# Optimization experiments

Measured on AMD Instinct MI355X. Metric: run time of the kernel, lower is better.

Reference implementation:

```python
import jax, jax.numpy as jnp
import numpy as np


def setup_inputs() -> dict:
    key = jax.random.key(0)
    ks = jax.random.split(key, 5)
    B, C, H, W = 16, 512, 64, 64
    cm = cn = C // 4  # int(C*0.5*0.5)
    # kaiming_normal fan_out for 1x1 conv: std = sqrt(2 / out_channels)
    def kaiming(k, out_c, in_c):
        return jax.random.normal(k, (out_c, in_c), jnp.float32) * np.sqrt(2.0 / out_c)
    return {
        "x": jax.random.normal(ks[0], (B, C, H, W), jnp.float32),
        "WA": kaiming(ks[1], cm, C), "bA": jnp.zeros((cm,), jnp.float32),
        "WB": kaiming(ks[2], cn, C), "bB": jnp.zeros((cn,), jnp.float32),
        "WV": kaiming(ks[3], cn, C), "bV": jnp.zeros((cn,), jnp.float32),
        "WR": kaiming(ks[4], C, cm), "bR": jnp.zeros((C,), jnp.float32),
    }


def reference(x, WA, bA, WB, bB, WV, bV, WR, bR):
    b, c, h, w = x.shape
    n = h * w
    xf = x.reshape(b, c, n)  # [b, c, n] flattened spatial
    # 1x1 convs == per-pixel GEMMs
    A = jnp.einsum('mc,bcn->bmn', WA, xf) + bA[None, :, None]          # [b, cm, n]
    Bm = jax.nn.softmax(jnp.einsum('mc,bcn->bmn', WB, xf) + bB[None, :, None], axis=1)  # softmax over channels
    Vm = jax.nn.softmax(jnp.einsum('mc,bcn->bmn', WV, xf) + bV[None, :, None], axis=1)
    # second-order pooling: global descriptors [b, cm, cn]
    gd = jnp.einsum('bmn,bkn->bmk', A, Bm)
    # distribute: [b, cm, n]
    Z = jnp.einsum('bmk,bkn->bmn', gd, Vm)
    # reconstruct 1x1 conv back to c channels
    out = jnp.einsum('cm,bmn->bcn', WR, Z) + bR[None, :, None]
    return out.reshape(b, c, h, w)
```

## Files before the change

### kernel.cpp

```cpp
#include <hip/hip_runtime.h>
#include <hip/hip_fp16.h>


typedef _Float16 half8 __attribute__((ext_vector_type(8)));
typedef float f32x4 __attribute__((ext_vector_type(4)));

__device__ __forceinline__ unsigned short f2h(float v) {
  return __builtin_bit_cast(unsigned short, (_Float16)v);
}
__device__ __forceinline__ unsigned pk2(float a, float b) {
  return (unsigned)f2h(a) | ((unsigned)f2h(b) << 16);
}
__device__ __forceinline__ f32x4 mfma16(half8 a, half8 b, f32x4 c) {
  return __builtin_amdgcn_mfma_f32_16x16x32_f16(a, b, c, 0, 0, 0);
}
__device__ __forceinline__ int perm32(int v) {
  return (((v & 15) >> 2) << 3) | (((v >> 4) & 1) << 2) | (v & 3);
}
__device__ __forceinline__ void glds16(const unsigned short* g, unsigned short* l) {
  __builtin_amdgcn_global_load_lds(
      (const __attribute__((address_space(1))) unsigned int*)g,
      (__attribute__((address_space(3))) unsigned int*)l, 16, 0, 0);
}
__device__ __forceinline__ half8 ld_frag(const unsigned short* lds, int row) {
  int kg = (threadIdx.x & 63) >> 4;
  uint4 u = *(const uint4*)&lds[(kg * 128 + row) * 8];
  return __builtin_bit_cast(half8, u);
}
__device__ __forceinline__ half8 ld_frag64(const unsigned short* lds, int row) {
  int kg = (threadIdx.x & 63) >> 4;
  uint4 u = *(const uint4*)&lds[(kg * 64 + row) * 8];
  return __builtin_bit_cast(half8, u);
}

__device__ __forceinline__ void stage_glds256(unsigned short* lds,
                                              const unsigned short* g,
                                              int gs, int k0) {
  const int lane = threadIdx.x & 63;
  const int w = threadIdx.x >> 6;
#pragma unroll
  for (int p = 0; p < 2; ++p) {
    int g0 = (w + p * 4) * 64;
    int gi = g0 + lane;
    int row = gi & 127, kg = gi >> 7;
    glds16(g + (size_t)row * gs + k0 + kg * 8, lds + g0 * 8);
  }
}

__global__ __launch_bounds__(256) void k_prep(
    const float* __restrict__ WA, const float* __restrict__ WB,
    const float* __restrict__ WV, const float* __restrict__ WR,
    unsigned short* __restrict__ Wh, unsigned short* __restrict__ WRh) {
  int idx = blockIdx.x * 256 + threadIdx.x;
  if (idx < 196608) {
    int mg = idx >> 16, r = idx & 65535;
    const float* src = (mg == 0) ? WA : ((mg == 1) ? WB : WV);
    Wh[(idx & ~31) | perm32(idx & 31)] = f2h(src[r]);
  } else {
    int r = idx - 196608;
    WRh[(r & ~31) | perm32(r & 31)] = f2h(WR[r]);
  }
}

__global__ __launch_bounds__(384, 3) void k_abv_gd(
    const float* __restrict__ x, const unsigned short* __restrict__ Wh,
    const float* __restrict__ bA, const float* __restrict__ bB,
    const float* __restrict__ bV,
    unsigned short* __restrict__ VmT, float* __restrict__ gdP) {
  const int nt = blockIdx.x, b = blockIdx.y;
  const int tid = threadIdx.x, lane = tid & 63, w = tid >> 6;
  const int kg = lane >> 4, lidx = lane & 15;
  const int mg = w >> 1, wh = w & 1;

  __shared__ unsigned short smem[16384];
  __shared__ float cmaxs[2][2][64], csums[2][2][64];
  __shared__ float sBias[384];

  sBias[tid] = ((mg == 0) ? bA : ((mg == 1) ? bB : bV))[tid & 127];

  const float* xbase = x + (size_t)b * 512 * 4096 + nt * 64;
  const int xn = tid & 63;
  const int xkg = (tid >> 6) & 3;
  const bool xact = (tid < 256);

  float xr[8];

#define XLOAD(K0) do { \
  if (xact) { \
    _Pragma("unroll") for (int j = 0; j < 4; ++j) { \
      xr[j]     = xbase[(size_t)((K0) + 4 * xkg + j) * 4096 + xn]; \
      xr[4 + j] = xbase[(size_t)((K0) + 16 + 4 * xkg + j) * 4096 + xn]; \
    } } } while (0)

#define XWRITE(SX) do { \
  if (xact) { \
    uint4 u_; \
    u_.x = pk2(xr[0], xr[1]); u_.y = pk2(xr[2], xr[3]); \
    u_.z = pk2(xr[4], xr[5]); u_.w = pk2(xr[6], xr[7]); \
    *(uint4*)&(SX)[(xkg * 64 + xn) * 8] = u_; \
  } } while (0)

#define WLOAD(AF, K0) do { \
  _Pragma("unroll") for (int mf_ = 0; mf_ < 4; ++mf_) { \
    const unsigned short* wp_ = Wh + mg * 65536 + \
        (size_t)(wh * 64 + mf_ * 16 + lidx) * 512 + (K0) + kg * 8; \
    (AF)[mf_] = __builtin_bit_cast(half8, *(const uint4*)wp_); \
  } } while (0)

  f32x4 acc[4][4];
#pragma unroll
  for (int mf = 0; mf < 4; ++mf)
#pragma unroll
    for (int nf = 0; nf < 4; ++nf) acc[mf][nf] = (f32x4){0.f, 0.f, 0.f, 0.f};

  half8 afc[4], afn[4];

  XLOAD(0);
  WLOAD(afc, 0);
  XWRITE(smem);

  for (int ks = 0; ks < 16; ++ks) {
    unsigned short* cw = smem + (ks & 1) * 2048;
    unsigned short* nx = smem + ((ks & 1) ^ 1) * 2048;
    __syncthreads();
    if (ks < 15) {
      XLOAD((ks + 1) * 32);
      WLOAD(afn, (ks + 1) * 32);
    }
#pragma unroll
    for (int nf = 0; nf < 4; ++nf) {
      half8 bf = ld_frag64(cw, nf * 16 + lidx);
#pragma unroll
      for (int mf = 0; mf < 4; ++mf)
        acc[mf][nf] = mfma16(afc[mf], bf, acc[mf][nf]);
    }
    if (ks < 15) {
      XWRITE(nx);
#pragma unroll
      for (int mf = 0; mf < 4; ++mf) afc[mf] = afn[mf];
    }
  }

#pragma unroll
  for (int mf = 0; mf < 4; ++mf)
#pragma unroll
    for (int i = 0; i < 4; ++i) {
      float bb = sBias[mg * 128 + wh * 64 + mf * 16 + kg * 4 + i];
#pragma unroll
      for (int nf = 0; nf < 4; ++nf) acc[mf][nf][i] += bb;
    }

  float inv_s[4];
  if (mg) {
#pragma unroll
    for (int nf = 0; nf < 4; ++nf) {
      float m = -1e30f;
#pragma unroll
      for (int mf = 0; mf < 4; ++mf)
#pragma unroll
        for (int i = 0; i < 4; ++i) m = fmaxf(m, acc[mf][nf][i]);
      m = fmaxf(m, __shfl_xor(m, 16));
      m = fmaxf(m, __shfl_xor(m, 32));
      if (kg == 0) cmaxs[mg - 1][wh][nf * 16 + lidx] = m;
      inv_s[nf] = m;
    }
  }
  __syncthreads();
  if (mg) {
#pragma unroll
    for (int nf = 0; nf < 4; ++nf) {
      float m = fmaxf(inv_s[nf], cmaxs[mg - 1][wh ^ 1][nf * 16 + lidx]);
      float s = 0.f;
#pragma unroll
      for (int mf = 0; mf < 4; ++mf)
#pragma unroll
        for (int i = 0; i < 4; ++i) {
          float e = __expf(acc[mf][nf][i] - m);
          acc[mf][nf][i] = e;
          s += e;
        }
      s += __shfl_xor(s, 16);
      s += __shfl_xor(s, 32);
      if (kg == 0) csums[mg - 1][wh][nf * 16 + lidx] = s;
      inv_s[nf] = s;
    }
  }
  __syncthreads();
  if (mg) {
#pragma unroll
    for (int nf = 0; nf < 4; ++nf)
      inv_s[nf] = 1.f / (inv_s[nf] + csums[mg - 1][wh ^ 1][nf * 16 + lidx]);
  }

  unsigned short* sA2 = smem;
  unsigned short* sB2 = smem + 8192;

  __syncthreads();
  if (mg != 2) {
    unsigned short* dst = (mg == 0) ? sA2 : sB2;
#pragma unroll
    for (int nf = 0; nf < 4; ++nf) {
      int base = (nf >> 1) * 4096 + (lidx >> 2) * 1024 + (nf & 1) * 4 + (lidx & 3);
#pragma unroll
      for (int mf = 0; mf < 4; ++mf)
#pragma unroll
        for (int i = 0; i < 4; ++i) {
          int m_ = wh * 64 + mf * 16 + kg * 4 + i;
          float v = acc[mf][nf][i];
          dst[base + m_ * 8] = f2h(mg ? v * inv_s[nf] : v);
        }
    }
  } else {
    const size_t vofs = ((size_t)b * 4096 + (size_t)nt * 64) * 128;
#pragma unroll
    for (int mf = 0; mf < 4; ++mf) {
      int m0 = wh * 64 + mf * 16 + kg * 4;
      int mp = (m0 & ~31) + perm32(m0 & 31);
#pragma unroll
      for (int nf = 0; nf < 4; ++nf) {
        int n_ = nf * 16 + lidx;
        ushort4 pk;
        pk.x = f2h(acc[mf][nf][0] * inv_s[nf]);
        pk.y = f2h(acc[mf][nf][1] * inv_s[nf]);
        pk.z = f2h(acc[mf][nf][2] * inv_s[nf]);
        pk.w = f2h(acc[mf][nf][3] * inv_s[nf]);
        *(ushort4*)&VmT[vofs + (size_t)n_ * 128 + mp] = pk;
      }
    }
  }
  __syncthreads();

  if (mg != 2) {
    const int gr = wh, gc = mg;
    f32x4 g2[4][4];
#pragma unroll
    for (int mf = 0; mf < 4; ++mf)
#pragma unroll
      for (int nf = 0; nf < 4; ++nf) g2[mf][nf] = (f32x4){0.f, 0.f, 0.f, 0.f};
#pragma unroll
    for (int ks2 = 0; ks2 < 2; ++ks2) {
      half8 af2[4];
#pragma unroll
      for (int mf = 0; mf < 4; ++mf)
        af2[mf] = ld_frag(sA2 + ks2 * 4096, gr * 64 + mf * 16 + lidx);
#pragma unroll
      for (int nf = 0; nf < 4; ++nf) {
        half8 bf2 = ld_frag(sB2 + ks2 * 4096, gc * 64 + nf * 16 + lidx);
#pragma unroll
        for (int mf = 0; mf < 4; ++mf)
          g2[mf][nf] = mfma16(af2[mf], bf2, g2[mf][nf]);
      }
    }
    float* gp = gdP + ((size_t)b * 64 + nt) * 16384;
#pragma unroll
    for (int mf = 0; mf < 4; ++mf)
#pragma unroll
      for (int nf = 0; nf < 4; ++nf) {
        int m0 = gr * 64 + mf * 16 + kg * 4;
        int k2 = gc * 64 + nf * 16 + lidx;
        *(f32x4*)&gp[(size_t)k2 * 128 + m0] = g2[mf][nf];
      }
  }
#undef XLOAD
#undef XWRITE
#undef WLOAD
}

__global__ __launch_bounds__(256) void k_gdred(
    const float* __restrict__ gdP, float* __restrict__ gdT) {
  int gid = blockIdx.x * 256 + threadIdx.x;
  int o = gid * 4;
  int b = o >> 14, rem = o & 16383;
  const float* src = gdP + (size_t)b * 64 * 16384 + rem;
  f32x4 s = (f32x4){0.f, 0.f, 0.f, 0.f};
#pragma unroll 8
  for (int nt = 0; nt < 64; ++nt) s += *(const f32x4*)(src + (size_t)nt * 16384);
  *(f32x4*)(gdT + o) = s;
}

__global__ __launch_bounds__(256) void k_gw(
    const float* __restrict__ gdT, const unsigned short* __restrict__ WRh,
    unsigned short* __restrict__ GWh) {
  const int ct = blockIdx.x, b = blockIdx.y;
  const int tid = threadIdx.x, lane = tid & 63;
  const int w = tid >> 6, wr = w >> 1, wc = w & 1;
  const int kg = lane >> 4, lidx = lane & 15;
  __shared__ unsigned short sG[4096], sWr[4096];
  const float* gb = gdT + (size_t)b * 16384;
  const unsigned short* Wb = WRh + ct * 128 * 128;

  f32x4 acc[4][4];
#pragma unroll
  for (int mf = 0; mf < 4; ++mf)
#pragma unroll
    for (int nf = 0; nf < 4; ++nf) acc[mf][nf] = (f32x4){0.f, 0.f, 0.f, 0.f};

  for (int k0 = 0; k0 < 128; k0 += 32) {
#pragma unroll
    for (int p = 0; p < 2; ++p) {
      int g = tid + p * 256;
      int row = g & 127, kgx = g >> 7;
      const float* s0 = &gb[row * 128 + k0 + 4 * kgx];
      float4 v0 = *(const float4*)s0;
      float4 v1 = *(const float4*)(s0 + 16);
      uint4 u;
      u.x = pk2(v0.x, v0.y); u.y = pk2(v0.z, v0.w);
      u.z = pk2(v1.x, v1.y); u.w = pk2(v1.z, v1.w);
      *(uint4*)&sG[g * 8] = u;
    }
    stage_glds256(sWr, Wb, 128, k0);
    __syncthreads();
    half8 af[4];
#pragma unroll
    for (int mf = 0; mf < 4; ++mf) af[mf] = ld_frag(sG, wr * 64 + mf * 16 + lidx);
#pragma unroll
    for (int nf = 0; nf < 4; ++nf) {
      half8 bf = ld_frag(sWr, wc * 64 + nf * 16 + lidx);
#pragma unroll
      for (int mf = 0; mf < 4; ++mf) acc[mf][nf] = mfma16(af[mf], bf, acc[mf][nf]);
    }
    __syncthreads();
  }
  const size_t gofs = ((size_t)b * 512 + (size_t)ct * 128) * 128;
#pragma unroll
  for (int mf = 0; mf < 4; ++mf) {
    int k0g = wr * 64 + mf * 16 + kg * 4;
    int kp = (k0g & ~31) + perm32(k0g & 31);
#pragma unroll
    for (int nf = 0; nf < 4; ++nf) {
      int c_ = wc * 64 + nf * 16 + lidx;
      ushort4 pk;
      pk.x = f2h(acc[mf][nf][0]); pk.y = f2h(acc[mf][nf][1]);
      pk.z = f2h(acc[mf][nf][2]); pk.w = f2h(acc[mf][nf][3]);
      *(ushort4*)&GWh[gofs + (size_t)c_ * 128 + kp] = pk;
    }
  }
}

__global__ __launch_bounds__(256) void k_out(
    const unsigned short* __restrict__ GWh, const unsigned short* __restrict__ VmT,
    const float* __restrict__ bR, float* __restrict__ out) {
  const int nt = blockIdx.x, ct = blockIdx.y, b = blockIdx.z;
  const int tid = threadIdx.x, lane = tid & 63;
  const int w = tid >> 6, wr = w >> 1, wc = w & 1;
  const int kg = lane >> 4, lidx = lane & 15;
  __shared__ unsigned short sW[4096], sZ[4096];
  __shared__ float sBias[128];
  if (tid < 128) sBias[tid] = bR[ct * 128 + tid];
  const unsigned short* Wb = GWh + ((size_t)b * 512 + (size_t)ct * 128) * 128;
  const unsigned short* Zb = VmT + ((size_t)b * 4096 + (size_t)nt * 128) * 128;

  f32x4 acc[4][4];
#pragma unroll
  for (int mf = 0; mf < 4; ++mf)
#pragma unroll
    for (int nf = 0; nf < 4; ++nf) acc[mf][nf] = (f32x4){0.f, 0.f, 0.f, 0.f};

  for (int k0 = 0; k0 < 128; k0 += 32) {
    stage_glds256(sW, Wb, 128, k0);
    stage_glds256(sZ, Zb, 128, k0);
    __syncthreads();
    half8 af[4];
#pragma unroll
    for (int mf = 0; mf < 4; ++mf) af[mf] = ld_frag(sW, wr * 64 + mf * 16 + lidx);
#pragma unroll
    for (int nf = 0; nf < 4; ++nf) {
      half8 bf = ld_frag(sZ, wc * 64 + nf * 16 + lidx);
#pragma unroll
      for (int mf = 0; mf < 4; ++mf) acc[mf][nf] = mfma16(af[mf], bf, acc[mf][nf]);
    }
    __syncthreads();
  }
#pragma unroll
  for (int mf = 0; mf < 4; ++mf)
#pragma unroll
    for (int nf = 0; nf < 4; ++nf)
#pragma unroll
      for (int i = 0; i < 4; ++i) {
        int cl = wr * 64 + mf * 16 + kg * 4 + i;
        int n_ = nt * 128 + wc * 64 + nf * 16 + lidx;
        out[((size_t)b * 512 + ct * 128 + cl) * 4096 + n_] = acc[mf][nf][i] + sBias[cl];
      }
}

extern "C" void kernel_launch(void* const* d_in, const int* in_sizes, int n_in,
                              void* d_out, int out_size, void* d_ws, size_t ws_size,
                              hipStream_t stream) {
  const float* x  = (const float*)d_in[0];
  const float* WA = (const float*)d_in[1];
  const float* bA = (const float*)d_in[2];
  const float* WB = (const float*)d_in[3];
  const float* bB = (const float*)d_in[4];
  const float* WV = (const float*)d_in[5];
  const float* bV = (const float*)d_in[6];
  const float* WR = (const float*)d_in[7];
  const float* bR = (const float*)d_in[8];
  float* out = (float*)d_out;

  char* ws = (char*)d_ws;
  unsigned short* Wh  = (unsigned short*)(ws);
  unsigned short* WRh = (unsigned short*)(ws + 393216);
  unsigned short* VmT = (unsigned short*)(ws + 524288);
  float*          gdT = (float*)(ws + 17301504);
  unsigned short* GWh = (unsigned short*)(ws + 18350080);
  float*          gdP = (float*)(ws + 20447232);

  k_prep<<<1024, 256, 0, stream>>>(WA, WB, WV, WR, Wh, WRh);
  k_abv_gd<<<dim3(64, 16), 384, 0, stream>>>(x, Wh, bA, bB, bV, VmT, gdP);
  k_gdred<<<256, 256, 0, stream>>>(gdP, gdT);
  k_gw<<<dim3(4, 16), 256, 0, stream>>>(gdT, WRh, GWh);
  k_out<<<dim3(32, 4, 16), 256, 0, stream>>>(GWh, VmT, bR, out);
}
```

Before: 182.9 us.

## Raise k_abv_gd occupancy, unroll K-loop by two, scalarize gd reduction

Raises the main GEMM kernel's launch bound to four blocks per CU. To fit the tighter register budget, the held-over weight fragments are dropped: weights are now loaded right before each MFMA step instead of being prefetched. The K loop is unrolled by two with alternating x staging registers. Separately, the partial-gd reduction switches from float4 to scalar per-thread sums over four times as many blocks, to spread the memory traffic more widely. The risks are exposed weight-load latency and possible register spills under the tighter bound.

After: 197.7 us. 1.08x slower.

```diff
diff --git a/kernel.cpp b/kernel.cpp
--- a/kernel.cpp
+++ b/kernel.cpp
@@ -62,7 +62,7 @@
   }
 }
 
-__global__ __launch_bounds__(384, 3) void k_abv_gd(
+__global__ __launch_bounds__(384, 4) void k_abv_gd(
     const float* __restrict__ x, const unsigned short* __restrict__ Wh,
     const float* __restrict__ bA, const float* __restrict__ bB,
     const float* __restrict__ bV,
@@ -83,28 +83,34 @@
   const int xkg = (tid >> 6) & 3;
   const bool xact = (tid < 256);
 
-  float xr[8];
-
-#define XLOAD(K0) do { \
+  float xrA[8], xrB[8];
+
+#define XLOAD(XR, K0) do { \
   if (xact) { \
     _Pragma("unroll") for (int j = 0; j < 4; ++j) { \
-      xr[j]     = xbase[(size_t)((K0) + 4 * xkg + j) * 4096 + xn]; \
-      xr[4 + j] = xbase[(size_t)((K0) + 16 + 4 * xkg + j) * 4096 + xn]; \
+      (XR)[j]     = xbase[(size_t)((K0) + 4 * xkg + j) * 4096 + xn]; \
+      (XR)[4 + j] = xbase[(size_t)((K0) + 16 + 4 * xkg + j) * 4096 + xn]; \
     } } } while (0)
 
-#define XWRITE(SX) do { \
+#define XWRITE(SX, XR) do { \
   if (xact) { \
     uint4 u_; \
-    u_.x = pk2(xr[0], xr[1]); u_.y = pk2(xr[2], xr[3]); \
-    u_.z = pk2(xr[4], xr[5]); u_.w = pk2(xr[6], xr[7]); \
+    u_.x = pk2((XR)[0], (XR)[1]); u_.y = pk2((XR)[2], (XR)[3]); \
+    u_.z = pk2((XR)[4], (XR)[5]); u_.w = pk2((XR)[6], (XR)[7]); \
     *(uint4*)&(SX)[(xkg * 64 + xn) * 8] = u_; \
   } } while (0)
 
-#define WLOAD(AF, K0) do { \
+#define MFMA_STEP(CW, K0) do { \
+  half8 af_[4]; \
   _Pragma("unroll") for (int mf_ = 0; mf_ < 4; ++mf_) { \
     const unsigned short* wp_ = Wh + mg * 65536 + \
         (size_t)(wh * 64 + mf_ * 16 + lidx) * 512 + (K0) + kg * 8; \
-    (AF)[mf_] = __builtin_bit_cast(half8, *(const uint4*)wp_); \
+    af_[mf_] = __builtin_bit_cast(half8, *(const uint4*)wp_); \
+  } \
+  _Pragma("unroll") for (int nf_ = 0; nf_ < 4; ++nf_) { \
+    half8 bf_ = ld_frag64((CW), nf_ * 16 + lidx); \
+    _Pragma("unroll") for (int mf_ = 0; mf_ < 4; ++mf_) \
+      acc[mf_][nf_] = mfma16(af_[mf_], bf_, acc[mf_][nf_]); \
   } } while (0)
 
   f32x4 acc[4][4];
@@ -113,32 +119,22 @@
 #pragma unroll
     for (int nf = 0; nf < 4; ++nf) acc[mf][nf] = (f32x4){0.f, 0.f, 0.f, 0.f};
 
-  half8 afc[4], afn[4];
-
-  XLOAD(0);
-  WLOAD(afc, 0);
-  XWRITE(smem);
-
-  for (int ks = 0; ks < 16; ++ks) {
-    unsigned short* cw = smem + (ks & 1) * 2048;
-    unsigned short* nx = smem + ((ks & 1) ^ 1) * 2048;
-    __syncthreads();
-    if (ks < 15) {
-      XLOAD((ks + 1) * 32);
-      WLOAD(afn, (ks + 1) * 32);
-    }
-#pragma unroll
-    for (int nf = 0; nf < 4; ++nf) {
-      half8 bf = ld_frag64(cw, nf * 16 + lidx);
-#pragma unroll
-      for (int mf = 0; mf < 4; ++mf)
-        acc[mf][nf] = mfma16(afc[mf], bf, acc[mf][nf]);
-    }
-    if (ks < 15) {
-      XWRITE(nx);
-#pragma unroll
-      for (int mf = 0; mf < 4; ++mf) afc[mf] = afn[mf];
-    }
+  unsigned short* buf0 = smem;
+  unsigned short* buf1 = smem + 2048;
+
+  XLOAD(xrA, 0);
+  XWRITE(buf0, xrA);
+  XLOAD(xrA, 32);
+
+  for (int ks = 0; ks < 16; ks += 2) {
+    __syncthreads();
+    if (ks < 14) XLOAD(xrB, (ks + 2) * 32);
+    MFMA_STEP(buf0, ks * 32);
+    XWRITE(buf1, xrA);
+    __syncthreads();
+    if (ks < 13) XLOAD(xrA, (ks + 3) * 32);
+    MFMA_STEP(buf1, (ks + 1) * 32);
+    if (ks < 14) XWRITE(buf0, xrB);
   }
 
 #pragma unroll
@@ -263,19 +259,18 @@
   }
 #undef XLOAD
 #undef XWRITE
-#undef WLOAD
+#undef MFMA_STEP
 }
 
 __global__ __launch_bounds__(256) void k_gdred(
     const float* __restrict__ gdP, float* __restrict__ gdT) {
   int gid = blockIdx.x * 256 + threadIdx.x;
-  int o = gid * 4;
-  int b = o >> 14, rem = o & 16383;
-  const float* src = gdP + (size_t)b * 64 * 16384 + rem;
-  f32x4 s = (f32x4){0.f, 0.f, 0.f, 0.f};
+  int b = gid >> 14, km = gid & 16383;
+  const float* src = gdP + (size_t)b * 64 * 16384 + km;
+  float s = 0.f;
 #pragma unroll 8
-  for (int nt = 0; nt < 64; ++nt) s += *(const f32x4*)(src + (size_t)nt * 16384);
-  *(f32x4*)(gdT + o) = s;
+  for (int nt = 0; nt < 64; ++nt) s += src[(size_t)nt * 16384];
+  gdT[gid] = s;
 }
 
 __global__ __launch_bounds__(256) void k_gw(
@@ -407,7 +402,7 @@
 
   k_prep<<<1024, 256, 0, stream>>>(WA, WB, WV, WR, Wh, WRh);
   k_abv_gd<<<dim3(64, 16), 384, 0, stream>>>(x, Wh, bA, bB, bV, VmT, gdP);
-  k_gdred<<<256, 256, 0, stream>>>(gdP, gdT);
+  k_gdred<<<1024, 256, 0, stream>>>(gdP, gdT);
   k_gw<<<dim3(4, 16), 256, 0, stream>>>(gdT, WRh, GWh);
   k_out<<<dim3(32, 4, 16), 256, 0, stream>>>(GWh, VmT, bR, out);
 }
```

## Stage fp32 x tiles via direct global-to-LDS loads with XOR swizzle

Applied to the files above, without the earlier changes.

The main projection kernel now copies fp32 x tiles straight into LDS with global_load_lds into a swizzled layout. It converts them to fp16 when reading MFMA fragments, replacing the register load, convert and LDS write path. Weight fragments are loaded per step without prefetch, and the occupancy hint rises to 4 blocks. The gd reduction kernel also switches from float4 to scalar per-thread work with 4x more blocks. The intent is to remove register staging and its pressure, at the cost of more LDS traffic and conversion work in the inner loop, plus weight load latency that is no longer hidden.

New measurement: 191.8 us, median of 2. +4.9%, slower.

```diff
diff --git a/kernel.cpp b/kernel.cpp
--- a/kernel.cpp
+++ b/kernel.cpp
@@ -17,7 +17,7 @@
 __device__ __forceinline__ int perm32(int v) {
   return (((v & 15) >> 2) << 3) | (((v >> 4) & 1) << 2) | (v & 3);
 }
-__device__ __forceinline__ void glds16(const unsigned short* g, unsigned short* l) {
+__device__ __forceinline__ void glds16(const void* g, void* l) {
   __builtin_amdgcn_global_load_lds(
       (const __attribute__((address_space(1))) unsigned int*)g,
       (__attribute__((address_space(3))) unsigned int*)l, 16, 0, 0);
@@ -27,9 +27,22 @@
   uint4 u = *(const uint4*)&lds[(kg * 128 + row) * 8];
   return __builtin_bit_cast(half8, u);
 }
-__device__ __forceinline__ half8 ld_frag64(const unsigned short* lds, int row) {
-  int kg = (threadIdx.x & 63) >> 4;
-  uint4 u = *(const uint4*)&lds[(kg * 64 + row) * 8];
+__device__ __forceinline__ half8 ld_frag_x32(const float* lds, int nf) {
+  const int lane = threadIdx.x & 63;
+  const int kg = lane >> 4, lidx = lane & 15;
+  const int q = nf * 4 + (lidx >> 2);
+  const int r = lidx & 3;
+  float v[8];
+#pragma unroll
+  for (int j = 0; j < 4; ++j) {
+    int c = 4 * kg + j;
+    int idx = c * 64 + (((q ^ c) & 15) << 2) + r;
+    v[j] = lds[idx];
+    v[4 + j] = lds[idx + 1024];
+  }
+  uint4 u;
+  u.x = pk2(v[0], v[1]); u.y = pk2(v[2], v[3]);
+  u.z = pk2(v[4], v[5]); u.w = pk2(v[6], v[7]);
   return __builtin_bit_cast(half8, u);
 }
 
@@ -62,7 +75,7 @@
   }
 }
 
-__global__ __launch_bounds__(384, 3) void k_abv_gd(
+__global__ __launch_bounds__(384, 4) void k_abv_gd(
     const float* __restrict__ x, const unsigned short* __restrict__ Wh,
     const float* __restrict__ bA, const float* __restrict__ bB,
     const float* __restrict__ bV,
@@ -72,39 +85,35 @@
   const int kg = lane >> 4, lidx = lane & 15;
   const int mg = w >> 1, wh = w & 1;
 
-  __shared__ unsigned short smem[16384];
+  __shared__ __align__(16) unsigned char smem_raw[32768];
+  float* xt0 = (float*)smem_raw;
+  float* xt1 = (float*)smem_raw + 2048;
+  unsigned short* sA2 = (unsigned short*)smem_raw;
+  unsigned short* sB2 = (unsigned short*)(smem_raw + 16384);
+
   __shared__ float cmaxs[2][2][64], csums[2][2][64];
   __shared__ float sBias[384];
 
   sBias[tid] = ((mg == 0) ? bA : ((mg == 1) ? bB : bV))[tid & 127];
 
   const float* xbase = x + (size_t)b * 512 * 4096 + nt * 64;
-  const int xn = tid & 63;
-  const int xkg = (tid >> 6) & 3;
-  const bool xact = (tid < 256);
-
-  float xr[8];
-
-#define XLOAD(K0) do { \
-  if (xact) { \
-    _Pragma("unroll") for (int j = 0; j < 4; ++j) { \
-      xr[j]     = xbase[(size_t)((K0) + 4 * xkg + j) * 4096 + xn]; \
-      xr[4 + j] = xbase[(size_t)((K0) + 16 + 4 * xkg + j) * 4096 + xn]; \
+
+#define XSTAGE(BUF, K0) do { \
+  if (tid < 256) { \
+    _Pragma("unroll") for (int p_ = 0; p_ < 2; ++p_) { \
+      int g0_ = (tid >> 6) * 64 + p_ * 256;    \
+      int s_ = g0_ + lane; \
+      int c_ = s_ >> 4; \
+      int q_ = (s_ & 15) ^ (c_ & 15); \
+      glds16(xbase + (size_t)((K0) + c_) * 4096 + q_ * 4, \
+             (float*)(BUF) + g0_ * 4); \
     } } } while (0)
 
-#define XWRITE(SX) do { \
-  if (xact) { \
-    uint4 u_; \
-    u_.x = pk2(xr[0], xr[1]); u_.y = pk2(xr[2], xr[3]); \
-    u_.z = pk2(xr[4], xr[5]); u_.w = pk2(xr[6], xr[7]); \
-    *(uint4*)&(SX)[(xkg * 64 + xn) * 8] = u_; \
-  } } while (0)
-
-#define WLOAD(AF, K0) do { \
+#define WLOAD(K0) do { \
   _Pragma("unroll") for (int mf_ = 0; mf_ < 4; ++mf_) { \
     const unsigned short* wp_ = Wh + mg * 65536 + \
         (size_t)(wh * 64 + mf_ * 16 + lidx) * 512 + (K0) + kg * 8; \
-    (AF)[mf_] = __builtin_bit_cast(half8, *(const uint4*)wp_); \
+    afc[mf_] = __builtin_bit_cast(half8, *(const uint4*)wp_); \
   } } while (0)
 
   f32x4 acc[4][4];
@@ -113,31 +122,21 @@
 #pragma unroll
     for (int nf = 0; nf < 4; ++nf) acc[mf][nf] = (f32x4){0.f, 0.f, 0.f, 0.f};
 
-  half8 afc[4], afn[4];
-
-  XLOAD(0);
-  WLOAD(afc, 0);
-  XWRITE(smem);
-
+  half8 afc[4];
+
+  XSTAGE(xt0, 0);
   for (int ks = 0; ks < 16; ++ks) {
-    unsigned short* cw = smem + (ks & 1) * 2048;
-    unsigned short* nx = smem + ((ks & 1) ^ 1) * 2048;
+    float* cw = (ks & 1) ? xt1 : xt0;
+    float* nx = (ks & 1) ? xt0 : xt1;
     __syncthreads();
-    if (ks < 15) {
-      XLOAD((ks + 1) * 32);
-      WLOAD(afn, (ks + 1) * 32);
-    }
-#pragma unroll
-    for (int nf = 0; nf < 4; ++nf) {
-      half8 bf = ld_frag64(cw, nf * 16 + lidx);
+    WLOAD(ks * 32);
+    if (ks < 15) XSTAGE(nx, (ks + 1) * 32);
+#pragma unroll
+    for (int nf = 0; nf < 4; ++nf) {
+      half8 bf = ld_frag_x32(cw, nf);
 #pragma unroll
       for (int mf = 0; mf < 4; ++mf)
         acc[mf][nf] = mfma16(afc[mf], bf, acc[mf][nf]);
-    }
-    if (ks < 15) {
-      XWRITE(nx);
-#pragma unroll
-      for (int mf = 0; mf < 4; ++mf) afc[mf] = afn[mf];
     }
   }
 
@@ -192,9 +191,6 @@
       inv_s[nf] = 1.f / (inv_s[nf] + csums[mg - 1][wh ^ 1][nf * 16 + lidx]);
   }
 
-  unsigned short* sA2 = smem;
-  unsigned short* sB2 = smem + 8192;
-
   __syncthreads();
   if (mg != 2) {
     unsigned short* dst = (mg == 0) ? sA2 : sB2;
@@ -261,21 +257,19 @@
         *(f32x4*)&gp[(size_t)k2 * 128 + m0] = g2[mf][nf];
       }
   }
-#undef XLOAD
-#undef XWRITE
+#undef XSTAGE
 #undef WLOAD
 }
 
 __global__ __launch_bounds__(256) void k_gdred(
     const float* __restrict__ gdP, float* __restrict__ gdT) {
   int gid = blockIdx.x * 256 + threadIdx.x;
-  int o = gid * 4;
-  int b = o >> 14, rem = o & 16383;
-  const float* src = gdP + (size_t)b * 64 * 16384 + rem;
-  f32x4 s = (f32x4){0.f, 0.f, 0.f, 0.f};
+  int b = gid >> 14, km = gid & 16383;
+  const float* src = gdP + (size_t)b * 64 * 16384 + km;
+  float s = 0.f;
 #pragma unroll 8
-  for (int nt = 0; nt < 64; ++nt) s += *(const f32x4*)(src + (size_t)nt * 16384);
-  *(f32x4*)(gdT + o) = s;
+  for (int nt = 0; nt < 64; ++nt) s += src[(size_t)nt * 16384];
+  gdT[gid] = s;
 }
 
 __global__ __launch_bounds__(256) void k_gw(
@@ -407,7 +401,7 @@
 
   k_prep<<<1024, 256, 0, stream>>>(WA, WB, WV, WR, Wh, WRh);
   k_abv_gd<<<dim3(64, 16), 384, 0, stream>>>(x, Wh, bA, bB, bV, VmT, gdP);
-  k_gdred<<<256, 256, 0, stream>>>(gdP, gdT);
+  k_gdred<<<1024, 256, 0, stream>>>(gdP, gdT);
   k_gw<<<dim3(4, 16), 256, 0, stream>>>(gdT, WRh, GWh);
   k_out<<<dim3(32, 4, 16), 256, 0, stream>>>(GWh, VmT, bR, out);
 }
```
